# Optimization experiments

Measured on AMD Instinct MI355X. Metric: run time of the kernel, lower is better.

The kernel has to match this reference:

```python
import jax, jax.numpy as jnp
import numpy as np

HEAD_NUM = 16
HEAD_DIM = 64
INPUT_DIM = 1024
OUTPUT_DIM = 1024
NEG_INF = -1e9  # value the torch code writes into masked score positions


def setup_inputs() -> dict:
    key = jax.random.key(0)
    k_x, k_v, k_w1, k_b1, k_w2, k_b2 = jax.random.split(key, 6)
    B, N = 2, 2048
    x = jax.random.normal(k_x, (B, N, INPUT_DIM), dtype=jnp.float32)
    vaild_num = jax.random.randint(k_v, (B,), 0, N, dtype=jnp.int32)
    s1 = 1.0 / np.sqrt(INPUT_DIM)
    s2 = 1.0 / np.sqrt(HEAD_NUM * HEAD_DIM)
    W_qkv = jax.random.uniform(k_w1, (INPUT_DIM, 3 * HEAD_NUM * HEAD_DIM), jnp.float32, -s1, s1)
    b_qkv = jax.random.uniform(k_b1, (3 * HEAD_NUM * HEAD_DIM,), jnp.float32, -s1, s1)
    W_proj = jax.random.uniform(k_w2, (HEAD_NUM * HEAD_DIM, OUTPUT_DIM), jnp.float32, -s2, s2)
    b_proj = jax.random.uniform(k_b2, (OUTPUT_DIM,), jnp.float32, -s2, s2)
    return {"x": x, "vaild_num": vaild_num, "W_qkv": W_qkv, "b_qkv": b_qkv,
            "W_proj": W_proj, "b_proj": b_proj}


def reference(x, vaild_num, W_qkv, b_qkv, W_proj, b_proj):
    B, N, _ = x.shape
    H, hd = HEAD_NUM, HEAD_DIM
    qkv = x @ W_qkv + b_qkv                      # [B, N, 3*H*hd]
    q, k, v = jnp.split(qkv, 3, axis=2)
    split = lambda t: t.reshape(B, N, H, hd).transpose(0, 2, 1, 3)  # [B, H, N, hd]
    q, k, v = split(q), split(k), split(v)
    score = jnp.einsum('bhqd,bhkd->bhqk', q, k) * (1.0 / np.sqrt(hd))
    # per-sample valid-length masking: rows >= v and cols >= v get -1e9
    valid = jnp.arange(N)[None, :] < vaild_num[:, None]            # [B, N]
    mask = valid[:, None, :, None] & valid[:, None, None, :]       # [B, 1, N, N]
    score = jnp.where(mask, score, NEG_INF)
    p = jax.nn.softmax(score, axis=-1)
    attn = jnp.einsum('bhqk,bhkd->bhqd', p, v)                     # [B, H, N, hd]
    attn = attn.transpose(0, 2, 1, 3).reshape(B, N, H * hd)
    return attn @ W_proj + b_proj
```

## Files before the change

### kernel.cpp

```cpp
#include <hip/hip_runtime.h>
#include <stdint.h>


typedef float    f32x4  __attribute__((ext_vector_type(4)));
typedef float    f32x16 __attribute__((ext_vector_type(16)));
typedef __bf16   bf16x8 __attribute__((ext_vector_type(8)));
typedef unsigned short u16x8 __attribute__((ext_vector_type(8)));
typedef unsigned int   u32x4 __attribute__((ext_vector_type(4)));
typedef unsigned short ushort_t;
typedef unsigned int   u32;

#define HEADS 16
#define HDIM  64
#define NTOK  2048
#define BATCH 2
#define DIN   1024
#define D3    3072
#define MTOT  4096

#define SC 0.18033688f

__device__ __forceinline__ ushort_t f2bf(float x) {
  uint32_t u = __builtin_bit_cast(uint32_t, x);
  uint32_t r = (u + 0x7fffu + ((u >> 16) & 1u)) >> 16;
  return (ushort_t)r;
}
__device__ __forceinline__ float bf2f(ushort_t u) {
  return __builtin_bit_cast(float, (uint32_t)u << 16);
}
__device__ __forceinline__ u32 cvt_pk_bf16(float lo, float hi) {
  u32 r;
  asm("v_cvt_pk_bf16_f32 %0, %1, %2" : "=v"(r) : "v"(lo), "v"(hi));
  return r;
}

__device__ __forceinline__ void gld_lds16(const void* g, void* l) {
  auto gp = reinterpret_cast<const __attribute__((address_space(1))) uint32_t*>(
      reinterpret_cast<uintptr_t>(g));
  auto lp = reinterpret_cast<__attribute__((address_space(3))) uint32_t*>(
      reinterpret_cast<uintptr_t>(l));
  __builtin_amdgcn_global_load_lds(gp, lp, 16, 0, 0);
}

__global__ __launch_bounds__(256) void conv_bf16_kernel(
    const float* __restrict__ in, ushort_t* __restrict__ out, int n) {
  int i = (blockIdx.x * 256 + threadIdx.x) * 8;
  if (i >= n) return;
  float4 a = *(const float4*)(in + i);
  float4 b = *(const float4*)(in + i + 4);
  u16x8 v;
  v[0]=f2bf(a.x); v[1]=f2bf(a.y); v[2]=f2bf(a.z); v[3]=f2bf(a.w);
  v[4]=f2bf(b.x); v[5]=f2bf(b.y); v[6]=f2bf(b.z); v[7]=f2bf(b.w);
  *(u16x8*)(out + i) = v;
}

__global__ __launch_bounds__(256) void transpose_bf16_kernel(
    const float* __restrict__ in, ushort_t* __restrict__ out, int R, int C) {
  __shared__ float tile[64][65];
  const int r0 = blockIdx.y * 64, c0 = blockIdx.x * 64;
  const int t = threadIdx.x;
#pragma unroll
  for (int it = 0; it < 4; ++it) {
    int r = it * 16 + (t >> 4);
    int c = (t & 15) * 4;
    float4 v = *(const float4*)(in + (size_t)(r0 + r) * C + c0 + c);
    tile[r][c] = v.x; tile[r][c+1] = v.y; tile[r][c+2] = v.z; tile[r][c+3] = v.w;
  }
  __syncthreads();
#pragma unroll
  for (int it = 0; it < 2; ++it) {
    int idx = it * 2048 + t * 8;
    int c = idx >> 6;
    int r = idx & 63;
    u16x8 v;
#pragma unroll
    for (int j = 0; j < 8; ++j) v[j] = f2bf(tile[r + j][c]);
    *(u16x8*)(out + (size_t)(c0 + c) * R + r0 + r) = v;
  }
}

__device__ __forceinline__ void gemm_tile_mainloop(
    const ushort_t* __restrict__ A, const ushort_t* __restrict__ Bt,
    const int K, const int m0, const int n0,
    ushort_t* aT, ushort_t* bT, f32x4 (&acc)[4][4]) {
  const int t = threadIdx.x;
  const int l = t & 63;
  const int wr = t >> 7;
  const int wc = (t >> 6) & 1;

#pragma unroll
  for (int mi = 0; mi < 4; ++mi)
#pragma unroll
    for (int ni = 0; ni < 4; ++ni) acc[mi][ni] = f32x4{0.f, 0.f, 0.f, 0.f};

  for (int k0 = 0; k0 < K; k0 += 64) {
#pragma unroll
    for (int c = 0; c < 4; ++c) {
      const int lin = c * 4096 + t * 16;
      const int row = lin >> 7;
      const int scb = (lin & 127) ^ ((row & 7) << 4);
      const int ldso = (c * 4096 + (t >> 6) * 1024) >> 1;
      gld_lds16(A + (size_t)(m0 + row) * K + k0 + (scb >> 1), aT + ldso);
      gld_lds16(Bt + (size_t)(n0 + row) * K + k0 + (scb >> 1), bT + ldso);
    }
    __syncthreads();
#pragma unroll
    for (int ks = 0; ks < 2; ++ks) {
      bf16x8 af[4], bfr[4];
#pragma unroll
      for (int mi = 0; mi < 4; ++mi) {
        const int row = wr * 64 + mi * 16 + (l & 15);
        const int cb = (((l >> 4) << 4) + (ks << 6)) ^ ((row & 7) << 4);
        af[mi] = *(const bf16x8*)((const char*)aT + row * 128 + cb);
      }
#pragma unroll
      for (int ni = 0; ni < 4; ++ni) {
        const int row = wc * 64 + ni * 16 + (l & 15);
        const int cb = (((l >> 4) << 4) + (ks << 6)) ^ ((row & 7) << 4);
        bfr[ni] = *(const bf16x8*)((const char*)bT + row * 128 + cb);
      }
#pragma unroll
      for (int mi = 0; mi < 4; ++mi)
#pragma unroll
        for (int ni = 0; ni < 4; ++ni)
          acc[mi][ni] = __builtin_amdgcn_mfma_f32_16x16x32_bf16(
              af[mi], bfr[ni], acc[mi][ni], 0, 0, 0);
    }
    __syncthreads();
  }
}

__global__ __launch_bounds__(256) void gemm_qkv_kernel(
    const ushort_t* __restrict__ xb, const ushort_t* __restrict__ wT,
    const float* __restrict__ bias,
    ushort_t* __restrict__ Qb, ushort_t* __restrict__ Kb, ushort_t* __restrict__ Vt) {
  __shared__ __align__(16) ushort_t aT[128 * 64];
  __shared__ __align__(16) ushort_t bT[128 * 64];
  f32x4 acc[4][4];
  const int m0 = blockIdx.y * 128, n0 = blockIdx.x * 128;
  gemm_tile_mainloop(xb, wT, DIN, m0, n0, aT, bT, acc);

  const int t = threadIdx.x, l = t & 63;
  const int wr = t >> 7, wc = (t >> 6) & 1;
  const int which = n0 >> 10;
#pragma unroll
  for (int mi = 0; mi < 4; ++mi) {
#pragma unroll
    for (int ni = 0; ni < 4; ++ni) {
      const int n = n0 + wc * 64 + ni * 16 + (l & 15);
      const int h = (n >> 6) & 15, d = n & 63;
      const float bv = bias[n];
#pragma unroll
      for (int i = 0; i < 4; ++i) {
        const int m = m0 + wr * 64 + mi * 16 + ((l >> 4) << 2) + i;
        const int b = m >> 11, tok = m & 2047;
        const ushort_t val = f2bf(acc[mi][ni][i] + bv);
        const size_t bh = (size_t)((b << 4) + h);
        if (which == 0)      Qb[(bh * NTOK + tok) * HDIM + d] = val;
        else if (which == 1) Kb[(bh * NTOK + tok) * HDIM + d] = val;
        else                 Vt[(bh * HDIM + d) * NTOK + tok] = val;
      }
    }
  }
}

__global__ __launch_bounds__(256) void gemm_proj_kernel(
    const ushort_t* __restrict__ ab, const ushort_t* __restrict__ wT,
    const float* __restrict__ bias, float* __restrict__ out) {
  __shared__ __align__(16) ushort_t aT[128 * 64];
  __shared__ __align__(16) ushort_t bT[128 * 64];
  f32x4 acc[4][4];
  const int m0 = blockIdx.y * 128, n0 = blockIdx.x * 128;
  gemm_tile_mainloop(ab, wT, DIN, m0, n0, aT, bT, acc);

  const int t = threadIdx.x, l = t & 63;
  const int wr = t >> 7, wc = (t >> 6) & 1;
#pragma unroll
  for (int mi = 0; mi < 4; ++mi) {
#pragma unroll
    for (int ni = 0; ni < 4; ++ni) {
      const int n = n0 + wc * 64 + ni * 16 + (l & 15);
      const float bv = bias[n];
#pragma unroll
      for (int i = 0; i < 4; ++i) {
        const int m = m0 + wr * 64 + mi * 16 + ((l >> 4) << 2) + i;
        out[(size_t)m * 1024 + n] = acc[mi][ni][i] + bv;
      }
    }
  }
}

__global__ __launch_bounds__(256) void vmean_kernel(
    const ushort_t* __restrict__ Vt, ushort_t* __restrict__ vmean) {
  const int row = blockIdx.x * 4 + (threadIdx.x >> 6);
  const int l = threadIdx.x & 63;
  const ushort_t* src = Vt + (size_t)row * NTOK;
  float s = 0.f;
#pragma unroll
  for (int j = 0; j < 4; ++j) {
    u16x8 v = *(const u16x8*)(src + ((j << 6) + l) * 8);
#pragma unroll
    for (int k = 0; k < 8; ++k) s += bf2f(v[k]);
  }
#pragma unroll
  for (int d2 = 1; d2 < 64; d2 <<= 1) s += __shfl_xor(s, d2);
  if (l == 0) vmean[row] = f2bf(s * (1.0f / 2048.0f));
}

__global__ __launch_bounds__(256) void attn_kernel(
    const ushort_t* __restrict__ Qb, const ushort_t* __restrict__ Kb,
    const ushort_t* __restrict__ Vt, const ushort_t* __restrict__ vmean,
    const int* __restrict__ validp, ushort_t* __restrict__ ob) {
  __shared__ ushort_t ot_all[4][32 * 68];

  const int h = blockIdx.y, b = blockIdx.z;
  const int valid = validp[b];
  const int t = threadIdx.x, w = t >> 6, l = t & 63;
  const int lq = l & 31, hi = l >> 5;
  const int wq0 = (blockIdx.x << 7) + (w << 5);
  const size_t bh = (size_t)((b << 4) + h);
  const ushort_t* Qp = Qb + bh * (NTOK * HDIM);
  const ushort_t* Kp = Kb + bh * (NTOK * HDIM);
  const ushort_t* Vp = Vt + bh * (HDIM * NTOK);

  f32x16 oacc[2];
#pragma unroll
  for (int db = 0; db < 2; ++db)
#pragma unroll
    for (int r = 0; r < 16; ++r) oacc[db][r] = 0.f;
  float m_run = -INFINITY, lsum = 0.f;

  if (wq0 < valid) {
    bf16x8 qf[4];
    const ushort_t* qbase = Qp + (size_t)(wq0 + lq) * HDIM + (hi << 3);
#pragma unroll
    for (int ks = 0; ks < 4; ++ks) qf[ks] = *(const bf16x8*)(qbase + (ks << 4));

    const int nt = (valid + 63) >> 6;
    for (int tt = 0; tt < nt; ++tt) {
      const int kv0 = tt << 6;

      bf16x8 kf[2][4];
#pragma unroll
      for (int kb2 = 0; kb2 < 2; ++kb2) {
        const ushort_t* kbase = Kp + (size_t)(kv0 + (kb2 << 5) + lq) * HDIM + (hi << 3);
#pragma unroll
        for (int ks = 0; ks < 4; ++ks) kf[kb2][ks] = *(const bf16x8*)(kbase + (ks << 4));
      }
      bf16x8 vf[2][2][2];
#pragma unroll
      for (int db = 0; db < 2; ++db) {
        const ushort_t* vbase = Vp + (size_t)((db << 5) + lq) * NTOK + kv0 + (hi << 3);
#pragma unroll
        for (int kb2 = 0; kb2 < 2; ++kb2)
#pragma unroll
          for (int k2 = 0; k2 < 2; ++k2)
            vf[db][kb2][k2] = *(const bf16x8*)(vbase + (kb2 << 5) + (k2 << 4));
      }

      f32x16 st[2];
#pragma unroll
      for (int kb2 = 0; kb2 < 2; ++kb2)
#pragma unroll
        for (int r = 0; r < 16; ++r) st[kb2][r] = 0.f;
      __builtin_amdgcn_s_setprio(1);
#pragma unroll
      for (int ks = 0; ks < 4; ++ks) {
        st[0] = __builtin_amdgcn_mfma_f32_32x32x16_bf16(kf[0][ks], qf[ks], st[0], 0, 0, 0);
        st[1] = __builtin_amdgcn_mfma_f32_32x32x16_bf16(kf[1][ks], qf[ks], st[1], 0, 0, 0);
      }
      __builtin_amdgcn_s_setprio(0);

      if (kv0 + 64 > valid) {
#pragma unroll
        for (int kb2 = 0; kb2 < 2; ++kb2)
#pragma unroll
          for (int r = 0; r < 16; ++r) {
            const int k = kv0 + (kb2 << 5) + (r & 3) + ((r >> 2) << 3) + (hi << 2);
            if (k >= valid) st[kb2][r] = -1e30f;
          }
      }

      float pm;
      {
        float a8[8];
#pragma unroll
        for (int i = 0; i < 8; ++i)
          a8[i] = fmaxf(fmaxf(st[0][i], st[0][i + 8]), fmaxf(st[1][i], st[1][i + 8]));
        float b4[4];
#pragma unroll
        for (int i = 0; i < 4; ++i) b4[i] = fmaxf(a8[i], a8[i + 4]);
        pm = fmaxf(fmaxf(b4[0], b4[1]), fmaxf(b4[2], b4[3]));
      }
      pm = fmaxf(pm, __shfl_xor(pm, 32));

      if (__any(pm > m_run)) {
        const float mnew = fmaxf(m_run, pm);
        const float rs = exp2f((m_run - mnew) * SC);
        lsum *= rs;
#pragma unroll
        for (int db = 0; db < 2; ++db)
#pragma unroll
          for (int r = 0; r < 16; ++r) oacc[db][r] *= rs;
        m_run = mnew;
      }

      const float mc = m_run * SC;
      float pp[2][16];
      float ts4[4] = {0.f, 0.f, 0.f, 0.f};
#pragma unroll
      for (int kb2 = 0; kb2 < 2; ++kb2)
#pragma unroll
        for (int r = 0; r < 16; ++r) {
          const float e = exp2f(fmaf(st[kb2][r], SC, -mc));
          pp[kb2][r] = e;
          ts4[r & 3] += e;
        }
      float tsum = (ts4[0] + ts4[1]) + (ts4[2] + ts4[3]);
      tsum += __shfl_xor(tsum, 32);
      lsum += tsum;

      bf16x8 pb[2][2];
#pragma unroll
      for (int kb2 = 0; kb2 < 2; ++kb2) {
        u32 c[8];
#pragma unroll
        for (int m2 = 0; m2 < 8; ++m2)
          c[m2] = cvt_pk_bf16(pp[kb2][2 * m2], pp[kb2][2 * m2 + 1]);
        const u32 x1 = (u32)__shfl_xor((int)(hi ? c[0] : c[2]), 32);
        const u32 x2 = (u32)__shfl_xor((int)(hi ? c[1] : c[3]), 32);
        const u32 x3 = (u32)__shfl_xor((int)(hi ? c[4] : c[6]), 32);
        const u32 x4 = (u32)__shfl_xor((int)(hi ? c[5] : c[7]), 32);
        u32x4 w0, w1;
        w0[0] = hi ? x1 : c[0];  w0[1] = hi ? x2 : c[1];
        w0[2] = hi ? c[2] : x1;  w0[3] = hi ? c[3] : x2;
        w1[0] = hi ? x3 : c[4];  w1[1] = hi ? x4 : c[5];
        w1[2] = hi ? c[6] : x3;  w1[3] = hi ? c[7] : x4;
        pb[kb2][0] = __builtin_bit_cast(bf16x8, w0);
        pb[kb2][1] = __builtin_bit_cast(bf16x8, w1);
      }

      __builtin_amdgcn_s_setprio(1);
#pragma unroll
      for (int db = 0; db < 2; ++db)
#pragma unroll
        for (int kb2 = 0; kb2 < 2; ++kb2)
#pragma unroll
          for (int k2 = 0; k2 < 2; ++k2)
            oacc[db] = __builtin_amdgcn_mfma_f32_32x32x16_bf16(
                vf[db][kb2][k2], pb[kb2][k2], oacc[db], 0, 0, 0);
      __builtin_amdgcn_s_setprio(0);
    }
  }

  const float inv = (lsum > 0.f) ? 1.0f / lsum : 0.f;
  ushort_t* ot = ot_all[w];
#pragma unroll
  for (int db = 0; db < 2; ++db)
#pragma unroll
    for (int r = 0; r < 16; ++r) {
      const int d = (r & 3) + ((r >> 2) << 3) + (hi << 2) + (db << 5);
      ot[lq * 68 + d] = f2bf(oacc[db][r] * inv);
    }
  asm volatile("s_waitcnt lgkmcnt(0)" ::: "memory");
#pragma unroll
  for (int it = 0; it < 8; ++it) {
    const int c2 = it * 64 + l;
    const int row = c2 >> 4;
    const int ch = c2 & 15;
    const uint2 vo = *(const uint2*)((const char*)ot + row * 136 + ch * 8);
    const uint2 vm = *(const uint2*)(vmean + (bh << 6) + ch * 4);
    const int grow = wq0 + row;
    const uint2 sel = (grow < valid) ? vo : vm;
    *(uint2*)(ob + ((size_t)(b * NTOK) + grow) * 1024 + (h << 6) + ch * 4) = sel;
  }
}

extern "C" void kernel_launch(void* const* d_in, const int* in_sizes, int n_in,
                              void* d_out, int out_size, void* d_ws, size_t ws_size,
                              hipStream_t stream) {
  (void)in_sizes; (void)n_in; (void)out_size; (void)ws_size;
  const float* x      = (const float*)d_in[0];
  const int*   validp = (const int*)d_in[1];
  const float* W_qkv  = (const float*)d_in[2];
  const float* b_qkv  = (const float*)d_in[3];
  const float* W_proj = (const float*)d_in[4];
  const float* b_proj = (const float*)d_in[5];
  float* out = (float*)d_out;

  ushort_t* xb     = (ushort_t*)d_ws;
  ushort_t* wqkvT  = xb + 4194304;
  ushort_t* wprojT = wqkvT + 3145728;
  ushort_t* Qb     = wprojT + 1048576;
  ushort_t* Kb     = Qb + 4194304;
  ushort_t* Vt     = Kb + 4194304;
  ushort_t* ab     = Vt + 4194304;
  ushort_t* vm     = ab + 4194304;

  conv_bf16_kernel<<<2048, 256, 0, stream>>>(x, xb, 4194304);
  transpose_bf16_kernel<<<dim3(48, 16), 256, 0, stream>>>(W_qkv, wqkvT, 1024, 3072);
  transpose_bf16_kernel<<<dim3(16, 16), 256, 0, stream>>>(W_proj, wprojT, 1024, 1024);
  gemm_qkv_kernel<<<dim3(24, 32), 256, 0, stream>>>(xb, wqkvT, b_qkv, Qb, Kb, Vt);
  vmean_kernel<<<512, 256, 0, stream>>>(Vt, vm);
  attn_kernel<<<dim3(16, 16, 2), 256, 0, stream>>>(Qb, Kb, Vt, vm, validp, ab);
  gemm_proj_kernel<<<dim3(8, 32), 256, 0, stream>>>(ab, wprojT, b_proj, out);
}
```

Before: 246.2 us.

## Stage K/V tiles in swizzled shared memory with double buffering

The attention kernel now loads each 64-key K and V tile once per block into LDS, using direct global-to-LDS loads and an XOR swizzle, and double-buffers the tiles. Previously each of the four waves fetched the same K/V tile from global memory on its own. The goal is to cut redundant global/L2 traffic and to overlap the next tile's load with the current tile's compute. The cost is a block-wide barrier on every tile, 32 KB of LDS per block, and idle waves whose query rows are invalid still having to take part in staging.

```diff
diff --git a/kernel.cpp b/kernel.cpp
--- a/kernel.cpp
+++ b/kernel.cpp
@@ -211,13 +211,14 @@
     const ushort_t* __restrict__ Qb, const ushort_t* __restrict__ Kb,
     const ushort_t* __restrict__ Vt, const ushort_t* __restrict__ vmean,
     const int* __restrict__ validp, ushort_t* __restrict__ ob) {
-  __shared__ ushort_t ot_all[4][32 * 68];
+  __shared__ __align__(16) char smem_raw[32768];
 
   const int h = blockIdx.y, b = blockIdx.z;
   const int valid = validp[b];
   const int t = threadIdx.x, w = t >> 6, l = t & 63;
   const int lq = l & 31, hi = l >> 5;
-  const int wq0 = (blockIdx.x << 7) + (w << 5);
+  const int bq0 = blockIdx.x << 7;
+  const int wq0 = bq0 + (w << 5);
   const size_t bh = (size_t)((b << 4) + h);
   const ushort_t* Qp = Qb + bh * (NTOK * HDIM);
   const ushort_t* Kp = Kb + bh * (NTOK * HDIM);
@@ -230,131 +231,163 @@
     for (int r = 0; r < 16; ++r) oacc[db][r] = 0.f;
   float m_run = -INFINITY, lsum = 0.f;
 
-  if (wq0 < valid) {
+  if (bq0 < valid) {
+    const bool qvalid = (wq0 < valid);
     bf16x8 qf[4];
-    const ushort_t* qbase = Qp + (size_t)(wq0 + lq) * HDIM + (hi << 3);
-#pragma unroll
-    for (int ks = 0; ks < 4; ++ks) qf[ks] = *(const bf16x8*)(qbase + (ks << 4));
+    if (qvalid) {
+      const ushort_t* qbase = Qp + (size_t)(wq0 + lq) * HDIM + (hi << 3);
+#pragma unroll
+      for (int ks = 0; ks < 4; ++ks) qf[ks] = *(const bf16x8*)(qbase + (ks << 4));
+    }
 
     const int nt = (valid + 63) >> 6;
+
+    auto STAGE = [&](int p, int kv0) {
+      char* kdst = smem_raw + p * 16384;
+      char* vdst = kdst + 8192;
+#pragma unroll
+      for (int c = 0; c < 2; ++c) {
+        const int lin = c * 4096 + t * 16;
+        const int row = lin >> 7;
+        const int scb = (lin & 127) ^ ((row & 7) << 4);
+        const int ldso = c * 4096 + (w << 10);
+        gld_lds16(Kp + (size_t)(kv0 + row) * HDIM + (scb >> 1), kdst + ldso);
+        gld_lds16(Vp + (size_t)row * NTOK + kv0 + (scb >> 1), vdst + ldso);
+      }
+    };
+
+    STAGE(0, 0);
+    __syncthreads();
+
     for (int tt = 0; tt < nt; ++tt) {
+      const int p = tt & 1;
       const int kv0 = tt << 6;
-
-      bf16x8 kf[2][4];
-#pragma unroll
-      for (int kb2 = 0; kb2 < 2; ++kb2) {
-        const ushort_t* kbase = Kp + (size_t)(kv0 + (kb2 << 5) + lq) * HDIM + (hi << 3);
-#pragma unroll
-        for (int ks = 0; ks < 4; ++ks) kf[kb2][ks] = *(const bf16x8*)(kbase + (ks << 4));
-      }
-      bf16x8 vf[2][2][2];
-#pragma unroll
-      for (int db = 0; db < 2; ++db) {
-        const ushort_t* vbase = Vp + (size_t)((db << 5) + lq) * NTOK + kv0 + (hi << 3);
+      if (tt + 1 < nt) STAGE(p ^ 1, (tt + 1) << 6);
+
+      if (qvalid) {
+        const char* kbuf = smem_raw + p * 16384;
+        const char* vbuf = kbuf + 8192;
+
+        bf16x8 kf[2][4];
+#pragma unroll
+        for (int kb2 = 0; kb2 < 2; ++kb2) {
+          const int row = (kb2 << 5) + lq;
+          const int sw = (row & 7) << 4;
+#pragma unroll
+          for (int ks = 0; ks < 4; ++ks)
+            kf[kb2][ks] = *(const bf16x8*)(kbuf + row * 128 + (((ks << 5) + (hi << 4)) ^ sw));
+        }
+
+        f32x16 st[2];
 #pragma unroll
         for (int kb2 = 0; kb2 < 2; ++kb2)
 #pragma unroll
-          for (int k2 = 0; k2 < 2; ++k2)
-            vf[db][kb2][k2] = *(const bf16x8*)(vbase + (kb2 << 5) + (k2 << 4));
-      }
-
-      f32x16 st[2];
-#pragma unroll
-      for (int kb2 = 0; kb2 < 2; ++kb2)
-#pragma unroll
-        for (int r = 0; r < 16; ++r) st[kb2][r] = 0.f;
-      __builtin_amdgcn_s_setprio(1);
-#pragma unroll
-      for (int ks = 0; ks < 4; ++ks) {
-        st[0] = __builtin_amdgcn_mfma_f32_32x32x16_bf16(kf[0][ks], qf[ks], st[0], 0, 0, 0);
-        st[1] = __builtin_amdgcn_mfma_f32_32x32x16_bf16(kf[1][ks], qf[ks], st[1], 0, 0, 0);
-      }
-      __builtin_amdgcn_s_setprio(0);
-
-      if (kv0 + 64 > valid) {
+          for (int r = 0; r < 16; ++r) st[kb2][r] = 0.f;
+        __builtin_amdgcn_s_setprio(1);
+#pragma unroll
+        for (int ks = 0; ks < 4; ++ks) {
+          st[0] = __builtin_amdgcn_mfma_f32_32x32x16_bf16(kf[0][ks], qf[ks], st[0], 0, 0, 0);
+          st[1] = __builtin_amdgcn_mfma_f32_32x32x16_bf16(kf[1][ks], qf[ks], st[1], 0, 0, 0);
+        }
+        __builtin_amdgcn_s_setprio(0);
+
+        if (kv0 + 64 > valid) {
+#pragma unroll
+          for (int kb2 = 0; kb2 < 2; ++kb2)
+#pragma unroll
+            for (int r = 0; r < 16; ++r) {
+              const int k = kv0 + (kb2 << 5) + (r & 3) + ((r >> 2) << 3) + (hi << 2);
+              if (k >= valid) st[kb2][r] = -1e30f;
+            }
+        }
+
+        float pm;
+        {
+          float a8[8];
+#pragma unroll
+          for (int i = 0; i < 8; ++i)
+            a8[i] = fmaxf(fmaxf(st[0][i], st[0][i + 8]), fmaxf(st[1][i], st[1][i + 8]));
+          float b4[4];
+#pragma unroll
+          for (int i = 0; i < 4; ++i) b4[i] = fmaxf(a8[i], a8[i + 4]);
+          pm = fmaxf(fmaxf(b4[0], b4[1]), fmaxf(b4[2], b4[3]));
+        }
+        pm = fmaxf(pm, __shfl_xor(pm, 32));
+
+        if (__any(pm > m_run)) {
+          const float mnew = fmaxf(m_run, pm);
+          const float rs = exp2f((m_run - mnew) * SC);
+          lsum *= rs;
+#pragma unroll
+          for (int db = 0; db < 2; ++db)
+#pragma unroll
+            for (int r = 0; r < 16; ++r) oacc[db][r] *= rs;
+          m_run = mnew;
+        }
+
+        const float mc = m_run * SC;
+        float pp[2][16];
+        float ts4[4] = {0.f, 0.f, 0.f, 0.f};
 #pragma unroll
         for (int kb2 = 0; kb2 < 2; ++kb2)
 #pragma unroll
           for (int r = 0; r < 16; ++r) {
-            const int k = kv0 + (kb2 << 5) + (r & 3) + ((r >> 2) << 3) + (hi << 2);
-            if (k >= valid) st[kb2][r] = -1e30f;
+            const float e = exp2f(fmaf(st[kb2][r], SC, -mc));
+            pp[kb2][r] = e;
+            ts4[r & 3] += e;
           }
-      }
-
-      float pm;
-      {
-        float a8[8];
-#pragma unroll
-        for (int i = 0; i < 8; ++i)
-          a8[i] = fmaxf(fmaxf(st[0][i], st[0][i + 8]), fmaxf(st[1][i], st[1][i + 8]));
-        float b4[4];
-#pragma unroll
-        for (int i = 0; i < 4; ++i) b4[i] = fmaxf(a8[i], a8[i + 4]);
-        pm = fmaxf(fmaxf(b4[0], b4[1]), fmaxf(b4[2], b4[3]));
-      }
-      pm = fmaxf(pm, __shfl_xor(pm, 32));
-
-      if (__any(pm > m_run)) {
-        const float mnew = fmaxf(m_run, pm);
-        const float rs = exp2f((m_run - mnew) * SC);
-        lsum *= rs;
+        float tsum = (ts4[0] + ts4[1]) + (ts4[2] + ts4[3]);
+        tsum += __shfl_xor(tsum, 32);
+        lsum += tsum;
+
+        bf16x8 vf[2][4];
+#pragma unroll
+        for (int db = 0; db < 2; ++db) {
+          const int row = (db << 5) + lq;
+          const int sw = (row & 7) << 4;
+#pragma unroll
+          for (int ks2 = 0; ks2 < 4; ++ks2)
+            vf[db][ks2] = *(const bf16x8*)(vbuf + row * 128 + (((ks2 << 5) + (hi << 4)) ^ sw));
+        }
+
+        bf16x8 pb[2][2];
+#pragma unroll
+        for (int kb2 = 0; kb2 < 2; ++kb2) {
+          u32 c[8];
+#pragma unroll
+          for (int m2 = 0; m2 < 8; ++m2)
+            c[m2] = cvt_pk_bf16(pp[kb2][2 * m2], pp[kb2][2 * m2 + 1]);
+          const u32 x1 = (u32)__shfl_xor((int)(hi ? c[0] : c[2]), 32);
+          const u32 x2 = (u32)__shfl_xor((int)(hi ? c[1] : c[3]), 32);
+          const u32 x3 = (u32)__shfl_xor((int)(hi ? c[4] : c[6]), 32);
+          const u32 x4 = (u32)__shfl_xor((int)(hi ? c[5] : c[7]), 32);
+          u32x4 w0, w1;
+          w0[0] = hi ? x1 : c[0];  w0[1] = hi ? x2 : c[1];
+          w0[2] = hi ? c[2] : x1;  w0[3] = hi ? c[3] : x2;
+          w1[0] = hi ? x3 : c[4];  w1[1] = hi ? x4 : c[5];
+          w1[2] = hi ? c[6] : x3;  w1[3] = hi ? c[7] : x4;
+          pb[kb2][0] = __builtin_bit_cast(bf16x8, w0);
+          pb[kb2][1] = __builtin_bit_cast(bf16x8, w1);
+        }
+
+        __builtin_amdgcn_s_setprio(1);
 #pragma unroll
         for (int db = 0; db < 2; ++db)
 #pragma unroll
-          for (int r = 0; r < 16; ++r) oacc[db][r] *= rs;
-        m_run = mnew;
-      }
-
-      const float mc = m_run * SC;
-      float pp[2][16];
-      float ts4[4] = {0.f, 0.f, 0.f, 0.f};
-#pragma unroll
-      for (int kb2 = 0; kb2 < 2; ++kb2)
-#pragma unroll
-        for (int r = 0; r < 16; ++r) {
-          const float e = exp2f(fmaf(st[kb2][r], SC, -mc));
-          pp[kb2][r] = e;
-          ts4[r & 3] += e;
-        }
-      float tsum = (ts4[0] + ts4[1]) + (ts4[2] + ts4[3]);
-      tsum += __shfl_xor(tsum, 32);
-      lsum += tsum;
-
-      bf16x8 pb[2][2];
-#pragma unroll
-      for (int kb2 = 0; kb2 < 2; ++kb2) {
-        u32 c[8];
-#pragma unroll
-        for (int m2 = 0; m2 < 8; ++m2)
-          c[m2] = cvt_pk_bf16(pp[kb2][2 * m2], pp[kb2][2 * m2 + 1]);
-        const u32 x1 = (u32)__shfl_xor((int)(hi ? c[0] : c[2]), 32);
-        const u32 x2 = (u32)__shfl_xor((int)(hi ? c[1] : c[3]), 32);
-        const u32 x3 = (u32)__shfl_xor((int)(hi ? c[4] : c[6]), 32);
-        const u32 x4 = (u32)__shfl_xor((int)(hi ? c[5] : c[7]), 32);
-        u32x4 w0, w1;
-        w0[0] = hi ? x1 : c[0];  w0[1] = hi ? x2 : c[1];
-        w0[2] = hi ? c[2] : x1;  w0[3] = hi ? c[3] : x2;
-        w1[0] = hi ? x3 : c[4];  w1[1] = hi ? x4 : c[5];
-        w1[2] = hi ? c[6] : x3;  w1[3] = hi ? c[7] : x4;
-        pb[kb2][0] = __builtin_bit_cast(bf16x8, w0);
-        pb[kb2][1] = __builtin_bit_cast(bf16x8, w1);
-      }
-
-      __builtin_amdgcn_s_setprio(1);
-#pragma unroll
-      for (int db = 0; db < 2; ++db)
-#pragma unroll
-        for (int kb2 = 0; kb2 < 2; ++kb2)
-#pragma unroll
-          for (int k2 = 0; k2 < 2; ++k2)
-            oacc[db] = __builtin_amdgcn_mfma_f32_32x32x16_bf16(
-                vf[db][kb2][k2], pb[kb2][k2], oacc[db], 0, 0, 0);
-      __builtin_amdgcn_s_setprio(0);
+          for (int kb2 = 0; kb2 < 2; ++kb2)
+#pragma unroll
+            for (int k2 = 0; k2 < 2; ++k2)
+              oacc[db] = __builtin_amdgcn_mfma_f32_32x32x16_bf16(
+                  vf[db][(kb2 << 1) + k2], pb[kb2][k2], oacc[db], 0, 0, 0);
+        __builtin_amdgcn_s_setprio(0);
+      }
+
+      __syncthreads();
     }
   }
 
   const float inv = (lsum > 0.f) ? 1.0f / lsum : 0.f;
-  ushort_t* ot = ot_all[w];
+  ushort_t* ot = (ushort_t*)smem_raw + w * (32 * 68);
 #pragma unroll
   for (int db = 0; db < 2; ++db)
 #pragma unroll
@@ -370,7 +403,7 @@
     const int ch = c2 & 15;
     const uint2 vo = *(const uint2*)((const char*)ot + row * 136 + ch * 8);
     const uint2 vm = *(const uint2*)(vmean + (bh << 6) + ch * 4);
-    const int grow = wq0 + row;
+    const int grow = (blockIdx.x << 7) + (w << 5) + row;
     const uint2 sel = (grow < valid) ? vo : vm;
     *(uint2*)(ob + ((size_t)(b * NTOK) + grow) * 1024 + (h << 6) + ch * 4) = sel;
   }
```

Measured after the change: 225.0 us. -8.6%, faster.
